# Kernel tuning notes

Hardware: AMD Instinct MI355X
Metric: run time of the kernel (lower is better)

The kernel has to match this reference:

```python
import jax, jax.numpy as jnp
import numpy as np

B, P, D = 64, 196, 2048      # batch, num_pixels, encoder_dim
E, H, A = 512, 512, 512      # embed, hidden, attention dims
V, S = 32000, 22             # vocab, caption seq_len


def setup_inputs() -> dict:
    key = jax.random.key(0)
    ks = jax.random.split(key, 24)
    sc = 0.02
    features = jax.random.normal(ks[0], (B, P, D), jnp.float32)
    captions = jax.random.randint(ks[1], (S, B), 0, V)
    caption_lengths = jax.random.randint(ks[2], (B,), 3, S + 1)
    caption_lengths = caption_lengths.at[0].set(S)  # make max static = S
    p = lambda i, shp: sc * jax.random.normal(ks[i], shp, jnp.float32)
    return {
        "features": features,
        "captions": captions,
        "caption_lengths": caption_lengths,
        "emb_W": p(3, (V, E)),
        "We": p(4, (D, A)), "be": p(5, (A,)),
        "Wd": p(6, (H, A)), "bd": p(7, (A,)),
        "wf": p(8, (A, 1)), "bf": p(9, (1,)),
        "Wih": p(10, (4 * H, E + D)), "Whh": p(11, (4 * H, H)),
        "bih": p(12, (4 * H,)), "bhh": p(13, (4 * H,)),
        "Wh0": p(14, (D, H)), "bh0": p(15, (H,)),
        "Wc0": p(16, (D, H)), "bc0": p(17, (H,)),
        "Wbeta": p(18, (H, D)), "bbeta": p(19, (D,)),
        "Wout": p(20, (H, V)), "bout": p(21, (V,)),
    }


def reference(features, captions, caption_lengths, emb_W, We, be, Wd, bd, wf, bf,
              Wih, Whh, bih, bhh, Wh0, bh0, Wc0, bc0, Wbeta, bbeta, Wout, bout):
    # sort batch by caption length, descending
    sort_ind = jnp.argsort(-caption_lengths)
    lens = caption_lengths[sort_ind]
    enc = features[sort_ind]                     # [B,P,D]
    caps = captions.T[sort_ind]                  # [B,S]
    emb = emb_W[caps]                            # [B,S,E]
    mean_enc = enc.mean(axis=1)
    h0 = mean_enc @ Wh0 + bh0
    c0 = mean_enc @ Wc0 + bc0
    decode_lengths = lens - 1
    T = captions.shape[0] - 2                    # max(decode_lengths) - 1, static
    att1 = enc @ We + be                         # [B,P,A], step-invariant
    emb_t = jnp.moveaxis(emb[:, :T, :], 1, 0)    # [T,B,E]
    t_idx = jnp.arange(T)

    def step(carry, inp):
        h, c = carry
        e_t, t = inp
        att2 = h @ Wd + bd                                   # [B,A]
        scores = (jax.nn.relu(att1 + att2[:, None, :]) @ wf)[..., 0] + bf[0]  # [B,P]
        alpha = jax.nn.softmax(scores, axis=1)
        awe = jnp.einsum('bpd,bp->bd', enc, alpha)           # [B,D]
        gate = jax.nn.sigmoid(h @ Wbeta + bbeta)             # [B,D]
        x = jnp.concatenate([e_t, gate * awe], axis=1)       # [B,E+D]
        g = x @ Wih.T + bih + h @ Whh.T + bhh                # [B,4H]
        i, f, gg, o = jnp.split(g, 4, axis=1)                # torch LSTMCell gate order
        c_new = jax.nn.sigmoid(f) * c + jax.nn.sigmoid(i) * jnp.tanh(gg)
        h_new = jax.nn.sigmoid(o) * jnp.tanh(c_new)
        preds = h_new @ Wout + bout                          # [B,V] (dropout in eval = identity)
        m = (decode_lengths > t)[:, None].astype(preds.dtype)
        return (h_new, c_new), (preds * m, alpha * m)

    (_, _), (preds, alphas) = jax.lax.scan(step, (h0, c0), (emb_t, t_idx))
    predictions = jnp.moveaxis(preds, 0, 1)   # [B,T,V]
    alphas = jnp.moveaxis(alphas, 0, 1)       # [B,T,P]
    return predictions, caps, lens, alphas, sort_ind
```

## Files before the change

kernel.cpp:

```cpp
#include <hip/hip_runtime.h>
#include <stdint.h>

typedef short s16x8 __attribute__((ext_vector_type(8)));
typedef short s16x4 __attribute__((ext_vector_type(4)));
typedef float f32x4 __attribute__((ext_vector_type(4)));
typedef unsigned short u16;
typedef unsigned int u32;

#define DEV __device__ __forceinline__

DEV float bf2f(u16 v){ union{float f; unsigned u;} x; x.u = ((unsigned)v)<<16; return x.f; }
DEV u16 f2bf(float f){ union{float f; unsigned u;} x; x.f = f; unsigned r = x.u + 0x7fffu + ((x.u>>16)&1u); return (u16)(r>>16); }
DEV float sigm(float x){ return 1.f/(1.f + __expf(-x)); }

DEV u32  aL(const u32* p){ return __hip_atomic_load(p, __ATOMIC_RELAXED, __HIP_MEMORY_SCOPE_AGENT); }
DEV void aS(u32* p, u32 v){ __hip_atomic_store(p, v, __ATOMIC_RELAXED, __HIP_MEMORY_SCOPE_AGENT); }
DEV float aLf(const float* p){ return __hip_atomic_load(p, __ATOMIC_RELAXED, __HIP_MEMORY_SCOPE_AGENT); }
DEV void aSf(float* p, float v){ __hip_atomic_store(p, v, __ATOMIC_RELAXED, __HIP_MEMORY_SCOPE_AGENT); }


enum { EPI_F32=0, EPI_BF16=1, EPI_H0C0=2, EPI_PREDS=3 };

struct EpiParams {
  float* out0; long ldo;
  u16* outb;
  const float* bias0;
  const int* declen;
  float* c; u16* xh;
};

template<int BM, int BN, int EPI, bool SWAPXY, int SWZM>
__global__ __launch_bounds__(256) void gemm_bt(
    const u16* __restrict__ A, long lda,
    const u16* __restrict__ B, long ldb,
    int K, EpiParams ep)
{
  constexpr int MF = BM/64;
  constexpr int NF = BN/16;
  constexpr int CHA = BM*8, CH = CHA + BN*8;
  constexpr int NST = CH/256;
  __shared__ char smem[(BM+BN)*128];
  const int tid = threadIdx.x;
  const int w = tid>>6, lane = tid&63;

  long arow0, brow0;
  if constexpr (SWZM > 0) {
    int id = blockIdx.x, tot = gridDim.x;
    int q = tot>>3, r = tot&7, xcd = id&7, idx = id>>3;
    int cid = (xcd<r) ? xcd*(q+1)+idx : r*(q+1)+(xcd-r)*q+idx;
    arow0 = (long)(cid % SWZM)*BM; brow0 = (long)(cid / SWZM)*BN;
  } else if constexpr (SWAPXY) { arow0 = (long)blockIdx.x*BM; brow0 = (long)blockIdx.y*BN; }
  else { arow0 = (long)blockIdx.y*BM; brow0 = (long)blockIdx.x*BN; }

  const u16* gsrc[NST]; int ldst[NST];
  #pragma unroll
  for (int i=0;i<NST;++i){
    int c = i*256 + tid;
    if (i*256 < CHA){
      int row = c>>3, k16 = c&7;
      gsrc[i] = A + (arow0+row)*lda + k16*8;
      ldst[i] = row*128 + ((k16*16) ^ ((row&7)<<4));
    } else {
      int cb = c - CHA; int row = cb>>3, k16 = cb&7;
      gsrc[i] = B + (brow0+row)*ldb + k16*8;
      ldst[i] = BM*128 + row*128 + ((k16*16) ^ ((row&7)<<4));
    }
  }

  f32x4 acc[MF][NF];
  #pragma unroll
  for (int i=0;i<MF;++i)
    #pragma unroll
    for (int j=0;j<NF;++j) acc[i][j] = (f32x4){0.f,0.f,0.f,0.f};

  const int KT = K >> 6;
  s16x8 st[NST];
  #pragma unroll
  for (int i=0;i<NST;++i) st[i] = *(const s16x8*)(gsrc[i]);

  char* Al = smem;
  for (int kk=0; kk<KT; ++kk){
    #pragma unroll
    for (int i=0;i<NST;++i) *(s16x8*)(smem + ldst[i]) = st[i];
    __syncthreads();
    if (kk+1 < KT){
      long kb = (long)(kk+1)*64;
      #pragma unroll
      for (int i=0;i<NST;++i) st[i] = *(const s16x8*)(gsrc[i] + kb);
    }
    #pragma unroll
    for (int ks = 0; ks < 2; ++ks) {
      s16x8 af[MF], bfr[NF];
      const int kboff = ks*64 + ((lane>>4)<<4);
      #pragma unroll
      for (int mf=0; mf<MF; ++mf) {
        int r = w*(16*MF) + mf*16 + (lane&15);
        af[mf] = *(const s16x8*)(Al + r*128 + (kboff ^ ((r&7)<<4)));
      }
      #pragma unroll
      for (int nf=0; nf<NF; ++nf) {
        int r = nf*16 + (lane&15);
        bfr[nf] = *(const s16x8*)(Al + BM*128 + r*128 + (kboff ^ ((r&7)<<4)));
      }
      #pragma unroll
      for (int mf=0; mf<MF; ++mf)
        #pragma unroll
        for (int nf=0; nf<NF; ++nf)
          acc[mf][nf] = __builtin_amdgcn_mfma_f32_16x16x32_bf16(bfr[nf], af[mf], acc[mf][nf], 0,0,0);
    }
    __syncthreads();
  }

  #pragma unroll
  for (int mf=0; mf<MF; ++mf)
    #pragma unroll
    for (int nf=0; nf<NF; ++nf){
      long m = arow0 + w*(16*MF) + mf*16 + (lane&15);
      long n0 = brow0 + nf*16 + ((lane>>4)<<2);
      f32x4 bv = *(const f32x4*)&ep.bias0[n0];
      f32x4 v = acc[mf][nf] + bv;
      if constexpr (EPI == EPI_F32) {
        *(f32x4*)&ep.out0[m*ep.ldo + n0] = v;
      } else if constexpr (EPI == EPI_BF16) {
        u16 o[4];
        #pragma unroll
        for (int r=0;r<4;++r) o[r] = f2bf(v[r]);
        *(s16x4*)&ep.outb[m*ep.ldo + n0] = *(s16x4*)o;
      } else if constexpr (EPI == EPI_H0C0) {
        if (n0 < 512){
          u16 o[4];
          #pragma unroll
          for (int r=0;r<4;++r) o[r] = f2bf(v[r]);
          *(s16x4*)&ep.xh[m*2560 + 2048 + n0] = *(s16x4*)o;
        } else {
          *(f32x4*)&ep.c[m*512 + (n0-512)] = v;
        }
      } else {
        int tt = (int)(m>>6), b = (int)(m&63);
        if (ep.declen[b] > tt)
          *(f32x4*)&ep.out0[(long)b*640000 + (long)tt*32000 + n0] = v;
      }
    }
}

DEV void gsync(u32* flags, u32* epochw, u32 ep, int blk, int tid){
  __syncthreads();
  if (blk == 0){
    if (tid == 0) aS(flags, ep);
    if (tid < 256){
      while (aL(flags + tid*16) < ep) __builtin_amdgcn_s_sleep(4);
    }
    __syncthreads();
    if (tid == 0) aS(epochw, ep);
  } else {
    if (tid == 0){
      aS(flags + blk*16, ep);
      while (aL(epochw) < ep) __builtin_amdgcn_s_sleep(8);
    }
    __syncthreads();
  }
}

struct FusedArgs {
  const u16* att1; const u16* enc;
  const u16* wmisc; const u16* wcat2;
  const float* gst; const float* wf; const float* bfp;
  const int* declen; const float* bmisc; const int* nact;
  u16* xh20; float* y0p;
  float* part; int* cnt; float* c; u16* hall;
  float* alph; u32* bar;
};

__global__ __launch_bounds__(512) void steps_fused(FusedArgs fa)
{
  __shared__ char smem[61440];
  __shared__ float wred[8];
  __shared__ int lastf;
  const int blk = blockIdx.x, tid = threadIdx.x;
  const int w = tid>>6, lane = tid&63;
  const int mstrip = w>>1, nhalf = w&1;
  u32* flags = fa.bar;
  u32* epochw = fa.bar + 4096;
  u32 ep = 0;

  for (int t=0; t<20; ++t){
    u16* cur = fa.xh20 + (long)t*163840;
    u16* nxt = cur + 163840;
    u32* cur32 = (u32*)cur;
    u32* nxt32 = (u32*)nxt;

    if (blk < 80){
      const int brow0 = blk*32;
      f32x4 acc = {0,0,0,0};
      #pragma unroll
      for (int r=0; r<2; ++r){
        u32 sa[16];
        #pragma unroll
        for (int i=0;i<16;++i){
          int c = i*512 + tid;
          int row = c>>7, kp = c&127;
          sa[i] = *(const u32*)(cur32 + (long)row*1280 + 1024 + r*128 + kp);
        }
        s16x8 sb[2];
        #pragma unroll
        for (int i=0;i<2;++i){
          int c = i*512 + tid;
          int row = c>>5, k16 = c&31;
          sb[i] = *(const s16x8*)(fa.wmisc + (long)(brow0+row)*512 + r*256 + k16*8);
        }
        #pragma unroll
        for (int i=0;i<16;++i){
          int c = i*512 + tid;
          int row = c>>7, kp = c&127;
          *(u32*)(smem + row*512 + ((kp*4) ^ ((row&7)<<4))) = sa[i];
        }
        #pragma unroll
        for (int i=0;i<2;++i){
          int c = i*512 + tid;
          int row = c>>5, k16 = c&31;
          *(s16x8*)(smem + 32768 + row*512 + ((k16*16) ^ ((row&7)<<4))) = sb[i];
        }
        __syncthreads();
        #pragma unroll
        for (int ks=0; ks<8; ++ks){
          int kboff = ks*64 + ((lane>>4)<<4);
          int ra = mstrip*16 + (lane&15);
          s16x8 af = *(const s16x8*)(smem + ra*512 + (kboff ^ ((ra&7)<<4)));
          int rb = nhalf*16 + (lane&15);
          s16x8 bf = *(const s16x8*)(smem + 32768 + rb*512 + (kboff ^ ((rb&7)<<4)));
          acc = __builtin_amdgcn_mfma_f32_16x16x32_bf16(bf, af, acc, 0,0,0);
        }
        __syncthreads();
      }
      int m = mstrip*16 + (lane&15);
      int n0 = brow0 + nhalf*16 + ((lane>>4)<<2);
      #pragma unroll
      for (int j=0;j<4;++j)
        aSf(fa.y0p + (long)m*2560 + n0 + j, acc[j] + fa.bmisc[n0+j]);
    }
    gsync(flags, epochw, ++ep, blk, tid);

    {
      const int b = blk & 63, s = blk >> 6;
      const int na = fa.nact[t];
      if (b >= na){
        if (s == 0){
          for (int i=tid; i<196; i+=512)
            fa.alph[((long)b*20 + t)*196 + i] = 0.f;
        }
      } else {
      float* att2p = (float*)smem;
      float* wfp   = att2p + 576;
      float* alps  = wfp + 576;
      float* awe_p = alps + 208;
      {
        int kg0 = tid>>6, j = tid&63;
        att2p[kg0*72 + j] = aLf(fa.y0p + (long)b*2560 + 2048 + tid);
        wfp[kg0*72 + j]   = fa.wf[tid];
      }
      __syncthreads();
      const float bfv = fa.bfp[0];
      const int pg = lane>>3, kg = lane&7;
      #pragma unroll
      for (int pass=0; pass<4; ++pass){
        int p = pass*64 + w*8 + pg;
        if (p < 196){
          const u16* ap = fa.att1 + (((long)(b*196 + p))<<9) + kg*64;
          float sa = 0.f;
          #pragma unroll
          for (int i=0;i<8;++i){
            s16x8 v = *(const s16x8*)(ap + i*8);
            #pragma unroll
            for (int q=0;q<8;++q){
              float x = bf2f((u16)v[q]) + att2p[kg*72 + i*8 + q];
              x = fmaxf(x, 0.f);
              sa += x * wfp[kg*72 + i*8 + q];
            }
          }
          sa += __shfl_xor(sa, 1);
          sa += __shfl_xor(sa, 2);
          sa += __shfl_xor(sa, 4);
          if (kg == 0) alps[p] = sa + bfv;
        }
      }
      __syncthreads();
      float v = (tid < 196) ? alps[tid] : -3.4e38f;
      float m8 = v;
      #pragma unroll
      for (int off=32; off; off>>=1) m8 = fmaxf(m8, __shfl_xor(m8, off));
      if (lane == 0) wred[w] = m8;
      __syncthreads();
      float mx = wred[0];
      #pragma unroll
      for (int i=1;i<8;++i) mx = fmaxf(mx, wred[i]);
      float e = (tid < 196) ? __expf(v - mx) : 0.f;
      float s8 = e;
      #pragma unroll
      for (int off=32; off; off>>=1) s8 += __shfl_xor(s8, off);
      __syncthreads();
      if (lane == 0) wred[w] = s8;
      __syncthreads();
      float den = wred[0]+wred[1]+wred[2]+wred[3]+wred[4]+wred[5]+wred[6]+wred[7];
      float inv = 1.f/den;
      if (tid < 196){
        float a = e*inv;
        alps[tid] = a;
        if (s==0) fa.alph[((long)b*20 + t)*196 + tid] = (fa.declen[b] > t) ? a : 0.f;
      }
      __syncthreads();
      const int d0 = s*512 + lane*8;
      const u16* ebase = fa.enc + (((long)b*196)<<11) + d0;
      float a8[8] = {0,0,0,0,0,0,0,0};
      int p = w;
      for (; p+24 < 196; p += 32){
        s16x8 e0 = __builtin_nontemporal_load((const s16x8*)(ebase + ((long)p<<11)));
        s16x8 e1 = __builtin_nontemporal_load((const s16x8*)(ebase + ((long)(p+8)<<11)));
        s16x8 e2 = __builtin_nontemporal_load((const s16x8*)(ebase + ((long)(p+16)<<11)));
        s16x8 e3 = __builtin_nontemporal_load((const s16x8*)(ebase + ((long)(p+24)<<11)));
        float a0 = alps[p], a1 = alps[p+8], a2 = alps[p+16], a3 = alps[p+24];
        #pragma unroll
        for (int q=0;q<8;++q) a8[q] += a0*bf2f((u16)e0[q]);
        #pragma unroll
        for (int q=0;q<8;++q) a8[q] += a1*bf2f((u16)e1[q]);
        #pragma unroll
        for (int q=0;q<8;++q) a8[q] += a2*bf2f((u16)e2[q]);
        #pragma unroll
        for (int q=0;q<8;++q) a8[q] += a3*bf2f((u16)e3[q]);
      }
      for (; p < 196; p += 8){
        s16x8 ev = __builtin_nontemporal_load((const s16x8*)(ebase + ((long)p<<11)));
        float a = alps[p];
        #pragma unroll
        for (int q=0;q<8;++q) a8[q] += a*bf2f((u16)ev[q]);
      }
      *(f32x4*)&awe_p[w*512 + lane*8]     = (f32x4){a8[0],a8[1],a8[2],a8[3]};
      *(f32x4*)&awe_p[w*512 + lane*8 + 4] = (f32x4){a8[4],a8[5],a8[6],a8[7]};
      __syncthreads();
      if (tid < 256){
        int c0 = 2*tid;
        float s0 = 0.f, s1 = 0.f;
        #pragma unroll
        for (int g=0; g<8; ++g){ s0 += awe_p[g*512 + c0]; s1 += awe_p[g*512 + c0 + 1]; }
        float g0 = sigm(aLf(fa.y0p + (long)b*2560 + s*512 + c0));
        float g1 = sigm(aLf(fa.y0p + (long)b*2560 + s*512 + c0 + 1));
        u32 pk = (u32)f2bf(g0*s0) | ((u32)f2bf(g1*s1) << 16);
        aS(cur32 + (long)b*1280 + s*256 + tid, pk);
      }
      __syncthreads();
      }
    }
    gsync(flags, epochw, ++ep, blk, tid);

    {
      const int ntile = blk & 63, split = blk >> 6;
      f32x4 acc = {0,0,0,0};
      #pragma unroll
      for (int r=0; r<2; ++r){
        const int kbw = split*640 + r*320;
        const int kbd = split*320 + r*160;
        u32 sa[20];
        #pragma unroll
        for (int i=0;i<20;++i){
          int c = i*512 + tid;
          int row = c/160, kp = c%160;
          sa[i] = *(const u32*)(cur32 + (long)row*1280 + kbd + kp);
        }
        s16x8 sb[3];
        #pragma unroll
        for (int i=0;i<3;++i){
          int c = i*512 + tid;
          if (c < 1280){
            int row = c/40, k16 = c%40;
            sb[i] = *(const s16x8*)(fa.wcat2 + (long)(ntile*32+row)*2560 + kbw + k16*8);
          }
        }
        #pragma unroll
        for (int i=0;i<20;++i){
          int c = i*512 + tid;
          int row = c/160, kp = c%160;
          *(u32*)(smem + row*640 + ((kp*4) ^ ((row&7)<<4))) = sa[i];
        }
        #pragma unroll
        for (int i=0;i<3;++i){
          int c = i*512 + tid;
          if (c < 1280){
            int row = c/40, k16 = c%40;
            *(s16x8*)(smem + 40960 + row*640 + ((k16*16) ^ ((row&7)<<4))) = sb[i];
          }
        }
        __syncthreads();
        #pragma unroll
        for (int ks=0; ks<10; ++ks){
          int kboff = ks*64 + ((lane>>4)<<4);
          int ra = mstrip*16 + (lane&15);
          s16x8 af = *(const s16x8*)(smem + ra*640 + (kboff ^ ((ra&7)<<4)));
          int rb = nhalf*16 + (lane&15);
          s16x8 bf = *(const s16x8*)(smem + 40960 + rb*640 + (kboff ^ ((rb&7)<<4)));
          acc = __builtin_amdgcn_mfma_f32_16x16x32_bf16(bf, af, acc, 0,0,0);
        }
        __syncthreads();
      }
      {
        float* PS = fa.part + (long)split*(64*2048);
        int m = mstrip*16 + (lane&15);
        int n0 = ntile*32 + nhalf*16 + ((lane>>4)<<2);
        #pragma unroll
        for (int j=0;j<4;++j) aSf(PS + (long)m*2048 + n0 + j, acc[j]);
      }
      __syncthreads();
      if (tid==0){
        int v = __hip_atomic_fetch_add(fa.cnt + t*64 + ntile, 1,
                                       __ATOMIC_RELAXED, __HIP_MEMORY_SCOPE_AGENT);
        lastf = (v == 3);
      }
      __syncthreads();
      if (lastf && tid < 256){
        int b = tid>>2, jp = tid&3;
        u16 h2[2];
        #pragma unroll
        for (int jj=0; jj<2; ++jj){
          int jl = jp*2 + jj;
          int j = ntile*8 + jl;
          float g4[4];
          #pragma unroll
          for (int gi=0; gi<4; ++gi){
            long n = (long)ntile*32 + jl*4 + gi;
            float sg = fa.gst[((long)t*64 + b)*2048 + n];
            #pragma unroll
            for (int sp=0; sp<4; ++sp)
              sg += aLf(fa.part + (long)sp*(64*2048) + (long)b*2048 + n);
            g4[gi] = sg;
          }
          float cc = aLf(fa.c + b*512 + j);
          float cn = sigm(g4[1])*cc + sigm(g4[0])*tanhf(g4[2]);
          float hn = sigm(g4[3])*tanhf(cn);
          aSf(fa.c + b*512 + j, cn);
          h2[jj] = f2bf(hn);
        }
        u32 pk = (u32)h2[0] | ((u32)h2[1] << 16);
        aS(nxt32 + (long)b*1280 + 1024 + ntile*4 + jp, pk);
        *(u32*)&fa.hall[((long)t*64 + b)*512 + ntile*8 + jp*2] = pk;
      }
    }
    if (t < 19) gsync(flags, epochw, ++ep, blk, tid);
  }
}

__global__ void sort_k(const int* __restrict__ cl, const int* __restrict__ captions,
                       int* __restrict__ sidx, int* __restrict__ declen,
                       float* __restrict__ outCaps, float* __restrict__ outLens,
                       float* __restrict__ outSidx, int* __restrict__ cnt,
                       u32* __restrict__ bar, int* __restrict__ nact)
{
  __shared__ int s_idx[64];
  __shared__ int s_dl[64];
  int i = threadIdx.x;
  int li = cl[i];
  int rank = 0;
  for (int j=0;j<64;++j){ int lj = cl[j]; rank += (lj>li) || (lj==li && j<i); }
  s_idx[rank] = i;
  __syncthreads();
  int src = s_idx[i];
  sidx[i] = src;
  int L = cl[src];
  declen[i] = L - 1;
  s_dl[i] = L - 1;
  outLens[i] = (float)L;
  outSidx[i] = (float)src;
  for (int s=0;s<22;++s) outCaps[i*22+s] = (float)captions[s*64 + src];
  for (int s=0;s<20;++s) cnt[s*64 + i] = 0;
  for (int s=i; s<4160; s+=64) bar[s] = 0u;
  __syncthreads();
  if (i < 20){
    int c = 0;
    for (int j=0;j<64;++j) c += (s_dl[j] > i);
    nact[i] = c;
  }
}

struct PrepArgs {
  const float* features; const int* captions; const int* sidx;
  const float* embW;
  const float* We; const float* Wbeta; const float* Wd;
  const float* Wh0; const float* Wc0; const float* Wout;
  const float* Wih; const float* Whh;
  const float* bih; const float* bhh; const float* bbeta;
  const float* bd; const float* bh0; const float* bc0;
  u16* enc; u16* meanb; u16* embb;
  u16* wet; u16* wmisc; u16* whc; u16* woutt; u16* wcat2; u16* wihe;
  float* bstat; float* bmisc; float* bhc;
};

DEV void tpose_tile(const float* __restrict__ in, u16* __restrict__ out,
                    int R, int C, int rel, int gx, float (*t)[65], int tid)
{
  const int bx = (rel % gx)*64, by = (rel / gx)*64;
  const int tx = tid & 63, ty = tid >> 6;
  #pragma unroll
  for (int i=0;i<16;++i){ int r = i*4+ty; t[r][tx] = in[(long)(by+r)*C + bx+tx]; }
  __syncthreads();
  #pragma unroll
  for (int i=0;i<16;++i){ int cc = i*4+ty; out[(long)(bx+cc)*R + by+tx] = f2bf(t[tx][cc]); }
}

__global__ __launch_bounds__(256) void mega_prep(PrepArgs pa)
{
  __shared__ float tls[64][65];
  __shared__ float red[4][256];
  const int blk = blockIdx.x, tid = threadIdx.x;

  if (blk < 512){
    int b = blk >> 3, oct = blk & 7;
    int lv = tid & 63, g = tid >> 6;
    int d0 = oct*256 + lv*4;
    const float* src = pa.features + (long)pa.sidx[b]*(196*2048) + d0;
    float acc[4] = {0.f,0.f,0.f,0.f};
    for (int p=g; p<196; p+=4){
      f32x4 v = *(const f32x4*)(src + (long)p*2048);
      u16 o[4];
      #pragma unroll
      for (int q=0;q<4;++q){ acc[q] += v[q]; o[q] = f2bf(v[q]); }
      *(s16x4*)(pa.enc + ((long)b*196 + p)*2048 + d0) = *(s16x4*)o;
    }
    #pragma unroll
    for (int q=0;q<4;++q) red[g][lv*4+q] = acc[q];
    __syncthreads();
    if (tid < 64){
      u16 mo[4];
      #pragma unroll
      for (int q=0;q<4;++q){
        float s = red[0][tid*4+q] + red[1][tid*4+q] + red[2][tid*4+q] + red[3][tid*4+q];
        mo[q] = f2bf(s*(1.f/196.f));
      }
      *(s16x4*)(pa.meanb + b*2048 + oct*256 + tid*4) = *(s16x4*)mo;
    }
  } else if (blk < 832){
    int idx = (blk-512)*256 + tid;
    int row = idx >> 6; int e0 = (idx & 63)*8;
    int t = row >> 6, b = row & 63;
    int tok = pa.captions[t*64 + pa.sidx[b]];
    const float* s = pa.embW + (long)tok*512 + e0;
    f32x4 v0 = *(const f32x4*)s, v1 = *(const f32x4*)(s+4);
    u16 o[8];
    #pragma unroll
    for (int q=0;q<4;++q){ o[q] = f2bf(v0[q]); o[4+q] = f2bf(v1[q]); }
    *(s16x8*)(pa.embb + (long)row*512 + e0) = *(s16x8*)o;
  } else if (blk < 4832){
    tpose_tile(pa.Wout, pa.woutt, 512, 32000, blk-832, 500, tls, tid);
  } else if (blk < 5088){
    tpose_tile(pa.We, pa.wet, 2048, 512, blk-4832, 8, tls, tid);
  } else if (blk < 5344){
    tpose_tile(pa.Wbeta, pa.wmisc, 512, 2048, blk-5088, 32, tls, tid);
  } else if (blk < 5408){
    tpose_tile(pa.Wd, pa.wmisc + 2048*512, 512, 512, blk-5344, 8, tls, tid);
  } else if (blk < 5664){
    tpose_tile(pa.Wh0, pa.whc, 2048, 512, blk-5408, 8, tls, tid);
  } else if (blk < 5920){
    tpose_tile(pa.Wc0, pa.whc + 512*2048, 2048, 512, blk-5664, 8, tls, tid);
  } else if (blk < 8480){
    long idx = (long)(blk-5920)*256 + tid;
    int r = (int)(idx / 320);
    int kc = (int)(idx % 320) * 8;
    int j = r>>2, g = r&3;
    int orow = g*512 + j;
    const float* s = (kc < 2048) ? (pa.Wih + (long)orow*2560 + 512 + kc)
                                 : (pa.Whh + (long)orow*512 + (kc - 2048));
    f32x4 v0 = *(const f32x4*)s, v1 = *(const f32x4*)(s+4);
    u16 o[8];
    #pragma unroll
    for (int q=0;q<4;++q){ o[q] = f2bf(v0[q]); o[4+q] = f2bf(v1[q]); }
    *(s16x8*)(pa.wcat2 + (long)r*2560 + kc) = *(s16x8*)o;
  } else if (blk < 8992){
    int idx = (blk-8480)*256 + tid;
    int r = idx >> 6; int kc = (idx & 63)*8;
    int j = r>>2, g = r&3;
    const float* s = pa.Wih + (long)(g*512+j)*2560 + kc;
    f32x4 v0 = *(const f32x4*)s, v1 = *(const f32x4*)(s+4);
    u16 o[8];
    #pragma unroll
    for (int q=0;q<4;++q){ o[q] = f2bf(v0[q]); o[4+q] = f2bf(v1[q]); }
    *(s16x8*)(pa.wihe + (long)r*512 + kc) = *(s16x8*)o;
  } else {
    int idx = (blk-8992)*256 + tid;
    if (idx < 2048){ int j = idx>>2, g = idx&3; pa.bstat[idx] = pa.bih[g*512+j] + pa.bhh[g*512+j]; }
    else if (idx < 4608){ int k = idx-2048; pa.bmisc[k] = (k<2048) ? pa.bbeta[k] : pa.bd[k-2048]; }
    else if (idx < 5632){ int k = idx-4608; pa.bhc[k] = (k<512) ? pa.bh0[k] : pa.bc0[k-512]; }
  }
}

static constexpr long OFF_ENC   = 0;
static constexpr long OFF_ATT1  = 51380224;
static constexpr long OFF_WOUTT = 64225280;
static constexpr long OFF_WET   = 96993280;
static constexpr long OFF_WMISC = 99090432;
static constexpr long OFF_WHC   = 101711872;
static constexpr long OFF_WCAT2 = 105906176;
static constexpr long OFF_WIHE  = 116391936;
static constexpr long OFF_EMBB  = 118489088;
static constexpr long OFF_GST   = 119799808;
static constexpr long OFF_HALL  = 130285568;
static constexpr long OFF_MEANB = 131596288;
static constexpr long OFF_C     = 132513792;
static constexpr long OFF_Y0P   = 132644864;
static constexpr long OFF_BSTAT = 133955584;
static constexpr long OFF_BMISC = 133963776;
static constexpr long OFF_BHC   = 133974016;
static constexpr long OFF_SIDX  = 133978112;
static constexpr long OFF_DECL  = 133978368;
static constexpr long OFF_CNT   = 133978624;
static constexpr long OFF_BAR   = 133983744;
static constexpr long OFF_NACT  = 134000384;
static constexpr long OFF_XH20  = 134017024;
static constexpr long OFF_PART  = OFF_WHC;

extern "C" void kernel_launch(void* const* d_in, const int* in_sizes, int n_in,
                              void* d_out, int out_size, void* d_ws, size_t ws_size,
                              hipStream_t stream)
{
  (void)in_sizes; (void)n_in; (void)out_size; (void)ws_size;
  const float* features = (const float*)d_in[0];
  const int*   captions = (const int*)d_in[1];
  const int*   caplen   = (const int*)d_in[2];
  const float* embW     = (const float*)d_in[3];
  const float* We       = (const float*)d_in[4];
  const float* be       = (const float*)d_in[5];
  const float* Wd       = (const float*)d_in[6];
  const float* bd       = (const float*)d_in[7];
  const float* wf       = (const float*)d_in[8];
  const float* bfp      = (const float*)d_in[9];
  const float* Wih      = (const float*)d_in[10];
  const float* Whh      = (const float*)d_in[11];
  const float* bih      = (const float*)d_in[12];
  const float* bhh      = (const float*)d_in[13];
  const float* Wh0      = (const float*)d_in[14];
  const float* bh0      = (const float*)d_in[15];
  const float* Wc0      = (const float*)d_in[16];
  const float* bc0      = (const float*)d_in[17];
  const float* Wbeta    = (const float*)d_in[18];
  const float* bbeta    = (const float*)d_in[19];
  const float* Wout     = (const float*)d_in[20];
  const float* bout     = (const float*)d_in[21];

  char* ws = (char*)d_ws;
  u16*   enc   = (u16*)(ws + OFF_ENC);
  u16*   att1  = (u16*)(ws + OFF_ATT1);
  u16*   woutt = (u16*)(ws + OFF_WOUTT);
  u16*   wet   = (u16*)(ws + OFF_WET);
  u16*   wmisc = (u16*)(ws + OFF_WMISC);
  u16*   whc   = (u16*)(ws + OFF_WHC);
  u16*   wcat2 = (u16*)(ws + OFF_WCAT2);
  u16*   wihe  = (u16*)(ws + OFF_WIHE);
  u16*   embb  = (u16*)(ws + OFF_EMBB);
  float* gst   = (float*)(ws + OFF_GST);
  u16*   hall  = (u16*)(ws + OFF_HALL);
  u16*   meanb = (u16*)(ws + OFF_MEANB);
  float* cbuf  = (float*)(ws + OFF_C);
  float* y0p   = (float*)(ws + OFF_Y0P);
  float* bstat = (float*)(ws + OFF_BSTAT);
  float* bmisc = (float*)(ws + OFF_BMISC);
  float* bhc   = (float*)(ws + OFF_BHC);
  int*   sidx  = (int*)(ws + OFF_SIDX);
  int*   declen= (int*)(ws + OFF_DECL);
  int*   cnt   = (int*)(ws + OFF_CNT);
  u32*   bar   = (u32*)(ws + OFF_BAR);
  int*   nact  = (int*)(ws + OFF_NACT);
  u16*   xh20  = (u16*)(ws + OFF_XH20);
  float* part  = (float*)(ws + OFF_PART);

  float* outP    = (float*)d_out;
  float* outCaps = outP + 40960000;
  float* outLens = outCaps + 1408;
  float* outAlph = outLens + 64;
  float* outSidx = outAlph + 250880;

  sort_k<<<1,64,0,stream>>>(caplen, captions, sidx, declen, outCaps, outLens, outSidx, cnt, bar, nact);
  {
    PrepArgs pa;
    pa.features = features; pa.captions = captions; pa.sidx = sidx;
    pa.embW = embW;
    pa.We = We; pa.Wbeta = Wbeta; pa.Wd = Wd; pa.Wh0 = Wh0; pa.Wc0 = Wc0; pa.Wout = Wout;
    pa.Wih = Wih; pa.Whh = Whh;
    pa.bih = bih; pa.bhh = bhh; pa.bbeta = bbeta; pa.bd = bd; pa.bh0 = bh0; pa.bc0 = bc0;
    pa.enc = enc; pa.meanb = meanb; pa.embb = embb;
    pa.wet = wet; pa.wmisc = wmisc; pa.whc = whc; pa.woutt = woutt;
    pa.wcat2 = wcat2; pa.wihe = wihe;
    pa.bstat = bstat; pa.bmisc = bmisc; pa.bhc = bhc;
    mega_prep<<<9014,256,0,stream>>>(pa);
  }

  { EpiParams ep{}; ep.bias0 = bhc; ep.xh = xh20; ep.c = cbuf;
    gemm_bt<64,64,EPI_H0C0,false,0><<<dim3(16,1),256,0,stream>>>(meanb, 2048, whc, 2048, 2048, ep); }
  { EpiParams ep{}; ep.outb = att1; ep.ldo = 512; ep.bias0 = be;
    gemm_bt<128,128,EPI_BF16,true,0><<<dim3(98,4),256,0,stream>>>(enc, 2048, wet, 2048, 2048, ep); }
  { EpiParams ep{}; ep.out0 = gst; ep.ldo = 2048; ep.bias0 = bstat;
    gemm_bt<128,64,EPI_F32,false,0><<<dim3(32,10),256,0,stream>>>(embb, 512, wihe, 512, 512, ep); }

  {
    FusedArgs fa;
    fa.att1 = att1; fa.enc = enc; fa.wmisc = wmisc; fa.wcat2 = wcat2;
    fa.gst = gst; fa.wf = wf; fa.bfp = bfp; fa.declen = declen; fa.bmisc = bmisc;
    fa.nact = nact;
    fa.xh20 = xh20; fa.y0p = y0p;
    fa.part = part; fa.cnt = cnt; fa.c = cbuf; fa.hall = hall;
    fa.alph = outAlph; fa.bar = bar;
    void* kargs[1] = { &fa };
    hipLaunchCooperativeKernel((const void*)steps_fused, dim3(256), dim3(512),
                               kargs, 0, stream);
  }

  { EpiParams ep{}; ep.out0 = outP; ep.bias0 = bout; ep.declen = declen;
    gemm_bt<128,128,EPI_PREDS,false,10><<<2500,256,0,stream>>>(hall, 512, woutt, 512, 512, ep); }
}
```

Baseline: 1.286 ms.

## Overlap Wout transpose with recurrent steps and merge setup GEMMs into one launch

The Wout transpose-to-bf16 moves out of the prep kernel and into the persistent fused step kernel. Blocks that are idle during the first phase of each timestep now transpose a slice of Wout, hiding that memory traffic behind the serial recurrence. The three setup GEMMs (h0/c0, att1, gates-static) are also merged into one launch with blockIdx-based dispatch, which removes launch gaps. The risk is that the extra work lengthens the critical path of each step if those blocks are not truly idle, and it adds pressure on memory bandwidth during the steps.

```diff
diff --git a/kernel.cpp b/kernel.cpp
--- a/kernel.cpp
+++ b/kernel.cpp
@@ -29,28 +29,17 @@
   float* c; u16* xh;
 };
 
-template<int BM, int BN, int EPI, bool SWAPXY, int SWZM>
-__global__ __launch_bounds__(256) void gemm_bt(
-    const u16* __restrict__ A, long lda,
-    const u16* __restrict__ B, long ldb,
-    int K, EpiParams ep)
+template<int BM, int BN, int EPI>
+DEV void gemm_core(const u16* __restrict__ A, long lda,
+                   const u16* __restrict__ B, long ldb,
+                   int K, EpiParams& ep, long arow0, long brow0,
+                   char* smem, int tid)
 {
   constexpr int MF = BM/64;
   constexpr int NF = BN/16;
   constexpr int CHA = BM*8, CH = CHA + BN*8;
   constexpr int NST = CH/256;
-  __shared__ char smem[(BM+BN)*128];
-  const int tid = threadIdx.x;
   const int w = tid>>6, lane = tid&63;
-
-  long arow0, brow0;
-  if constexpr (SWZM > 0) {
-    int id = blockIdx.x, tot = gridDim.x;
-    int q = tot>>3, r = tot&7, xcd = id&7, idx = id>>3;
-    int cid = (xcd<r) ? xcd*(q+1)+idx : r*(q+1)+(xcd-r)*q+idx;
-    arow0 = (long)(cid % SWZM)*BM; brow0 = (long)(cid / SWZM)*BN;
-  } else if constexpr (SWAPXY) { arow0 = (long)blockIdx.x*BM; brow0 = (long)blockIdx.y*BN; }
-  else { arow0 = (long)blockIdx.y*BM; brow0 = (long)blockIdx.x*BN; }
 
   const u16* gsrc[NST]; int ldst[NST];
   #pragma unroll
@@ -143,6 +132,46 @@
     }
 }
 
+template<int BM, int BN, int EPI, int SWZM>
+__global__ __launch_bounds__(256) void gemm_bt(
+    const u16* __restrict__ A, long lda,
+    const u16* __restrict__ B, long ldb,
+    int K, EpiParams ep)
+{
+  __shared__ char smem[(BM+BN)*128];
+  int id = blockIdx.x, tot = gridDim.x;
+  int q = tot>>3, r = tot&7, xcd = id&7, idx = id>>3;
+  int cid = (xcd<r) ? xcd*(q+1)+idx : r*(q+1)+(xcd-r)*q+idx;
+  long arow0 = (long)(cid % SWZM)*BM, brow0 = (long)(cid / SWZM)*BN;
+  gemm_core<BM,BN,EPI>(A, lda, B, ldb, K, ep, arow0, brow0, smem, threadIdx.x);
+}
+
+__global__ __launch_bounds__(256) void setup_gemms(
+    const u16* meanb, const u16* whc,
+    const u16* enc, const u16* wet,
+    const u16* embb, const u16* wihe,
+    u16* xh20, float* cbuf, const float* bhc,
+    u16* att1, const float* be,
+    float* gst, const float* bstat)
+{
+  __shared__ char smem[32768];
+  const int blk = blockIdx.x, tid = threadIdx.x;
+  if (blk < 16){
+    EpiParams ep{}; ep.bias0 = bhc; ep.xh = xh20; ep.c = cbuf;
+    gemm_core<64,64,EPI_H0C0>(meanb, 2048, whc, 2048, 2048, ep, 0, (long)blk*64, smem, tid);
+  } else if (blk < 408){
+    int rel = blk - 16;
+    EpiParams ep{}; ep.outb = att1; ep.ldo = 512; ep.bias0 = be;
+    gemm_core<128,128,EPI_BF16>(enc, 2048, wet, 2048, 2048, ep,
+                                (long)(rel % 98)*128, (long)(rel / 98)*128, smem, tid);
+  } else {
+    int rel = blk - 408;
+    EpiParams ep{}; ep.out0 = gst; ep.ldo = 2048; ep.bias0 = bstat;
+    gemm_core<128,64,EPI_F32>(embb, 512, wihe, 512, 512, ep,
+                              (long)(rel / 32)*128, (long)(rel % 32)*64, smem, tid);
+  }
+}
+
 DEV void gsync(u32* flags, u32* epochw, u32 ep, int blk, int tid){
   __syncthreads();
   if (blk == 0){
@@ -161,11 +190,25 @@
   }
 }
 
+DEV void tpose512(const float* __restrict__ in, u16* __restrict__ out,
+                  int R, int C, int rel, int gx, float (*t)[65], int tid)
+{
+  const int bx = (rel % gx)*64, by = (rel / gx)*64;
+  const int tx = tid & 63, ty = tid >> 6;
+  #pragma unroll
+  for (int i=0;i<8;++i){ int r = i*8+ty; t[r][tx] = in[(long)(by+r)*C + bx+tx]; }
+  __syncthreads();
+  #pragma unroll
+  for (int i=0;i<8;++i){ int cc = i*8+ty; out[(long)(bx+cc)*R + by+tx] = f2bf(t[tx][cc]); }
+  __syncthreads();
+}
+
 struct FusedArgs {
   const u16* att1; const u16* enc;
   const u16* wmisc; const u16* wcat2;
   const float* gst; const float* wf; const float* bfp;
   const int* declen; const float* bmisc; const int* nact;
+  const float* wout; u16* woutt;
   u16* xh20; float* y0p;
   float* part; int* cnt; float* c; u16* hall;
   float* alph; u32* bar;
@@ -237,6 +280,14 @@
       #pragma unroll
       for (int j=0;j<4;++j)
         aSf(fa.y0p + (long)m*2560 + n0 + j, acc[j] + fa.bmisc[n0+j]);
+    } else {
+      float (*tls)[65] = (float(*)[65])smem;
+      int base = t*352 + (blk-80)*2;
+      #pragma unroll
+      for (int k2=0;k2<2;++k2){
+        int rel = base + k2;
+        if (rel < 4000) tpose512(fa.wout, fa.woutt, 512, 32000, rel, 500, tls, tid);
+      }
     }
     gsync(flags, epochw, ++ep, blk, tid);
 
@@ -482,12 +533,12 @@
   const float* features; const int* captions; const int* sidx;
   const float* embW;
   const float* We; const float* Wbeta; const float* Wd;
-  const float* Wh0; const float* Wc0; const float* Wout;
+  const float* Wh0; const float* Wc0;
   const float* Wih; const float* Whh;
   const float* bih; const float* bhh; const float* bbeta;
   const float* bd; const float* bh0; const float* bc0;
   u16* enc; u16* meanb; u16* embb;
-  u16* wet; u16* wmisc; u16* whc; u16* woutt; u16* wcat2; u16* wihe;
+  u16* wet; u16* wmisc; u16* whc; u16* wcat2; u16* wihe;
   float* bstat; float* bmisc; float* bhc;
 };
 
@@ -545,20 +596,18 @@
     #pragma unroll
     for (int q=0;q<4;++q){ o[q] = f2bf(v0[q]); o[4+q] = f2bf(v1[q]); }
     *(s16x8*)(pa.embb + (long)row*512 + e0) = *(s16x8*)o;
-  } else if (blk < 4832){
-    tpose_tile(pa.Wout, pa.woutt, 512, 32000, blk-832, 500, tls, tid);
-  } else if (blk < 5088){
-    tpose_tile(pa.We, pa.wet, 2048, 512, blk-4832, 8, tls, tid);
-  } else if (blk < 5344){
-    tpose_tile(pa.Wbeta, pa.wmisc, 512, 2048, blk-5088, 32, tls, tid);
-  } else if (blk < 5408){
-    tpose_tile(pa.Wd, pa.wmisc + 2048*512, 512, 512, blk-5344, 8, tls, tid);
-  } else if (blk < 5664){
-    tpose_tile(pa.Wh0, pa.whc, 2048, 512, blk-5408, 8, tls, tid);
-  } else if (blk < 5920){
-    tpose_tile(pa.Wc0, pa.whc + 512*2048, 2048, 512, blk-5664, 8, tls, tid);
-  } else if (blk < 8480){
-    long idx = (long)(blk-5920)*256 + tid;
+  } else if (blk < 1088){
+    tpose_tile(pa.We, pa.wet, 2048, 512, blk-832, 8, tls, tid);
+  } else if (blk < 1344){
+    tpose_tile(pa.Wbeta, pa.wmisc, 512, 2048, blk-1088, 32, tls, tid);
+  } else if (blk < 1408){
+    tpose_tile(pa.Wd, pa.wmisc + 2048*512, 512, 512, blk-1344, 8, tls, tid);
+  } else if (blk < 1664){
+    tpose_tile(pa.Wh0, pa.whc, 2048, 512, blk-1408, 8, tls, tid);
+  } else if (blk < 1920){
+    tpose_tile(pa.Wc0, pa.whc + 512*2048, 2048, 512, blk-1664, 8, tls, tid);
+  } else if (blk < 4480){
+    long idx = (long)(blk-1920)*256 + tid;
     int r = (int)(idx / 320);
     int kc = (int)(idx % 320) * 8;
     int j = r>>2, g = r&3;
@@ -570,8 +619,8 @@
     #pragma unroll
     for (int q=0;q<4;++q){ o[q] = f2bf(v0[q]); o[4+q] = f2bf(v1[q]); }
     *(s16x8*)(pa.wcat2 + (long)r*2560 + kc) = *(s16x8*)o;
-  } else if (blk < 8992){
-    int idx = (blk-8480)*256 + tid;
+  } else if (blk < 4992){
+    int idx = (blk-4480)*256 + tid;
     int r = idx >> 6; int kc = (idx & 63)*8;
     int j = r>>2, g = r&3;
     const float* s = pa.Wih + (long)(g*512+j)*2560 + kc;
@@ -581,7 +630,7 @@
     for (int q=0;q<4;++q){ o[q] = f2bf(v0[q]); o[4+q] = f2bf(v1[q]); }
     *(s16x8*)(pa.wihe + (long)r*512 + kc) = *(s16x8*)o;
   } else {
-    int idx = (blk-8992)*256 + tid;
+    int idx = (blk-4992)*256 + tid;
     if (idx < 2048){ int j = idx>>2, g = idx&3; pa.bstat[idx] = pa.bih[g*512+j] + pa.bhh[g*512+j]; }
     else if (idx < 4608){ int k = idx-2048; pa.bmisc[k] = (k<2048) ? pa.bbeta[k] : pa.bd[k-2048]; }
     else if (idx < 5632){ int k = idx-4608; pa.bhc[k] = (k<512) ? pa.bh0[k] : pa.bc0[k-512]; }
@@ -678,28 +727,24 @@
     PrepArgs pa;
     pa.features = features; pa.captions = captions; pa.sidx = sidx;
     pa.embW = embW;
-    pa.We = We; pa.Wbeta = Wbeta; pa.Wd = Wd; pa.Wh0 = Wh0; pa.Wc0 = Wc0; pa.Wout = Wout;
+    pa.We = We; pa.Wbeta = Wbeta; pa.Wd = Wd; pa.Wh0 = Wh0; pa.Wc0 = Wc0;
     pa.Wih = Wih; pa.Whh = Whh;
     pa.bih = bih; pa.bhh = bhh; pa.bbeta = bbeta; pa.bd = bd; pa.bh0 = bh0; pa.bc0 = bc0;
     pa.enc = enc; pa.meanb = meanb; pa.embb = embb;
-    pa.wet = wet; pa.wmisc = wmisc; pa.whc = whc; pa.woutt = woutt;
+    pa.wet = wet; pa.wmisc = wmisc; pa.whc = whc;
     pa.wcat2 = wcat2; pa.wihe = wihe;
     pa.bstat = bstat; pa.bmisc = bmisc; pa.bhc = bhc;
-    mega_prep<<<9014,256,0,stream>>>(pa);
-  }
-
-  { EpiParams ep{}; ep.bias0 = bhc; ep.xh = xh20; ep.c = cbuf;
-    gemm_bt<64,64,EPI_H0C0,false,0><<<dim3(16,1),256,0,stream>>>(meanb, 2048, whc, 2048, 2048, ep); }
-  { EpiParams ep{}; ep.outb = att1; ep.ldo = 512; ep.bias0 = be;
-    gemm_bt<128,128,EPI_BF16,true,0><<<dim3(98,4),256,0,stream>>>(enc, 2048, wet, 2048, 2048, ep); }
-  { EpiParams ep{}; ep.out0 = gst; ep.ldo = 2048; ep.bias0 = bstat;
-    gemm_bt<128,64,EPI_F32,false,0><<<dim3(32,10),256,0,stream>>>(embb, 512, wihe, 512, 512, ep); }
+    mega_prep<<<5014,256,0,stream>>>(pa);
+  }
+  setup_gemms<<<728,256,0,stream>>>(meanb, whc, enc, wet, embb, wihe,
+                                    xh20, cbuf, bhc, att1, be, gst, bstat);
 
   {
     FusedArgs fa;
     fa.att1 = att1; fa.enc = enc; fa.wmisc = wmisc; fa.wcat2 = wcat2;
     fa.gst = gst; fa.wf = wf; fa.bfp = bfp; fa.declen = declen; fa.bmisc = bmisc;
     fa.nact = nact;
+    fa.wout = Wout; fa.woutt = woutt;
     fa.xh20 = xh20; fa.y0p = y0p;
     fa.part = part; fa.cnt = cnt; fa.c = cbuf; fa.hall = hall;
     fa.alph = outAlph; fa.bar = bar;
@@ -709,5 +754,5 @@
   }
 
   { EpiParams ep{}; ep.out0 = outP; ep.bias0 = bout; ep.declen = declen;
-    gemm_bt<128,128,EPI_PREDS,false,10><<<2500,256,0,stream>>>(hall, 512, woutt, 512, 512, ep); }
-}
+    gemm_bt<128,128,EPI_PREDS,10><<<2500,256,0,stream>>>(hall, 512, woutt, 512, 512, ep); }
+}
```

New measurement: 1.262 ms. Within noise of the previous version (-1.8%).
